# Kernel optimization log

Hardware: AMD Instinct MI355X
Metric: run time of the kernel (lower is better)

## Reference

```python
import jax, jax.numpy as jnp
import numpy as np

NEG_INF = -1e30  # stands in for -inf on the H-diagonal (matches softmax zeroing)


def conv1x1(x, W, b):
    # x: [B,C,H,W], W: [O,C], b: [O] -> [B,O,H,W]
    return jnp.einsum('bchw,oc->bohw', x, W) + b[None, :, None, None]


def setup_inputs() -> dict:
    key = jax.random.key(0)
    ks = jax.random.split(key, 8)
    B, C, H, W = 4, 64, 256, 256
    C8 = C // 8
    s = 1.0 / np.sqrt(C)
    return {
        'x': jax.random.normal(ks[0], (B, C, H, W), jnp.float32),
        'Wq': jax.random.normal(ks[1], (C8, C), jnp.float32) * s,
        'bq': jnp.zeros((C8,), jnp.float32),
        'Wk': jax.random.normal(ks[2], (C8, C), jnp.float32) * s,
        'bk': jnp.zeros((C8,), jnp.float32),
        'Wv': jax.random.normal(ks[3], (C, C), jnp.float32) * s,
        'bv': jnp.zeros((C,), jnp.float32),
        'gamma': jnp.zeros((1,), jnp.float32),
    }


def reference(x, Wq, bq, Wk, bk, Wv, bv, gamma):
    B, C, H, W = x.shape
    q = conv1x1(x, Wq, bq)   # [B,C8,H,W]
    k = conv1x1(x, Wk, bk)   # [B,C8,H,W]
    v = conv1x1(x, Wv, bv)   # [B,C,H,W]

    # Row (height-axis) attention energies with -inf on the self (diagonal) entry.
    energy_H = jnp.einsum('bchw,bcjw->bhwj', q, k)               # [B,H,W,H]
    diag = jnp.eye(H, dtype=bool)[:, None, :]                    # [H,1,H]
    energy_H = jnp.where(diag[None], NEG_INF, energy_H)
    # Column (width-axis) attention energies.
    energy_W = jnp.einsum('bchw,bchj->bhwj', q, k)               # [B,H,W,W]

    att = jax.nn.softmax(jnp.concatenate([energy_H, energy_W], axis=3), axis=3)
    att_H, att_W = att[..., :H], att[..., H:]                    # [B,H,W,H], [B,H,W,W]

    out_H = jnp.einsum('bcjw,bhwj->bchw', v, att_H)
    out_W = jnp.einsum('bchj,bhwj->bchw', v, att_W)
    return gamma[0] * (out_H + out_W) + x
```

## Files before the change

### kernel.cpp

```cpp
#include <hip/hip_runtime.h>

#define Bn 4
#define Cn 64
#define Hn 256
#define Wn 256
#define HWn 65536

typedef unsigned int u32;
typedef __attribute__((ext_vector_type(8))) short bf16x8;
typedef __attribute__((ext_vector_type(4))) float f32x4;
typedef __attribute__((ext_vector_type(16))) float f32x16;

__device__ __forceinline__ unsigned short f2b(float f) {
    union { float f; unsigned u; } v; v.f = f;
    return (unsigned short)(v.u >> 16);
}
__device__ __forceinline__ float b2f(unsigned short s) {
    union { float f; unsigned u; } v; v.u = ((unsigned)s) << 16;
    return v.f;
}
__device__ __forceinline__ u32 cvtpk(float lo, float hi) {
    u32 r;
    asm("v_cvt_pk_bf16_f32 %0, %1, %2" : "=v"(r) : "v"(lo), "v"(hi));
    return r;
}
__device__ __forceinline__ void vswap(u32& a, u32& b) {
    asm volatile("v_permlane32_swap_b32 %0, %1" : "+v"(a), "+v"(b));
}
__device__ __forceinline__ float pair_other(float v, int lane) {
    union { float f; u32 u; } A; A.f = v;
    u32 a = A.u, b = A.u;
    vswap(a, b);
    union { u32 u; float f; } R; R.u = (lane < 32) ? b : a;
    return R.f;
}
__device__ __forceinline__ bf16x8 buildP(const float* p) {
    u32 A = cvtpk(p[0], p[1]), B = cvtpk(p[4], p[5]);
    u32 C = cvtpk(p[2], p[3]), D = cvtpk(p[6], p[7]);
    vswap(A, B); vswap(C, D);
    union { u32 w[4]; bf16x8 v; } u;
    u.w[0] = A; u.w[1] = C; u.w[2] = B; u.w[3] = D;
    return u.v;
}

__global__ __launch_bounds__(256) void k_proj(
    const float* __restrict__ x,
    const float* __restrict__ Wq, const float* __restrict__ bq,
    const float* __restrict__ Wk, const float* __restrict__ bk,
    const float* __restrict__ Wv, const float* __restrict__ bv,
    unsigned short* __restrict__ qbr, unsigned short* __restrict__ kbr,
    unsigned short* __restrict__ qbT, unsigned short* __restrict__ kbT,
    unsigned short* __restrict__ v_row)
{
    int t = threadIdx.x, lane = t & 63, wv = t >> 6;
    int bid = blockIdx.x, b = bid >> 8, h = bid & 255;
    int row16 = lane & 15, g = lane >> 4;

    bf16x8 Af[5][2];
    #pragma unroll
    for (int m = 0; m < 5; ++m) {
        const float* wrow;
        if (m == 0) wrow = (row16 < 8) ? (Wq + row16 * 64) : (Wk + (row16 - 8) * 64);
        else        wrow = Wv + (size_t)((m - 1) * 16 + row16) * 64;
        #pragma unroll
        for (int ks = 0; ks < 2; ++ks) {
            int c0 = ks * 32 + g * 8;
            f32x4 w0 = *(const f32x4*)(wrow + c0);
            f32x4 w1 = *(const f32x4*)(wrow + c0 + 4);
            bf16x8 a;
            a[0] = (short)f2b(w0[0]); a[1] = (short)f2b(w0[1]);
            a[2] = (short)f2b(w0[2]); a[3] = (short)f2b(w0[3]);
            a[4] = (short)f2b(w1[0]); a[5] = (short)f2b(w1[1]);
            a[6] = (short)f2b(w1[2]); a[7] = (short)f2b(w1[3]);
            Af[m][ks] = a;
        }
    }

    f32x4 acc[5][4];
    #pragma unroll
    for (int m = 0; m < 5; ++m)
        #pragma unroll
        for (int nt = 0; nt < 4; ++nt)
            acc[m][nt] = (f32x4){0.f, 0.f, 0.f, 0.f};

    const float* xb = x + (size_t)b * Cn * HWn + (size_t)h * Wn;
    #pragma unroll
    for (int nt = 0; nt < 4; ++nt) {
        int p = wv * 64 + nt * 16 + row16;
        #pragma unroll
        for (int ks = 0; ks < 2; ++ks) {
            int c0 = ks * 32 + g * 8;
            bf16x8 bf;
            #pragma unroll
            for (int i = 0; i < 8; ++i)
                bf[i] = (short)f2b(xb[(size_t)(c0 + i) * HWn + p]);
            #pragma unroll
            for (int m = 0; m < 5; ++m)
                acc[m][nt] = __builtin_amdgcn_mfma_f32_16x16x32_bf16(Af[m][ks], bf, acc[m][nt], 0, 0, 0);
        }
    }

    f32x4 bQK = (g < 2) ? *(const f32x4*)(bq + g * 4)
                        : *(const f32x4*)(bk + (g - 2) * 4);
    #pragma unroll
    for (int nt = 0; nt < 4; ++nt) {
        int p = wv * 64 + nt * 16 + row16;
        f32x4 d = acc[0][nt];
        d[0] += bQK[0]; d[1] += bQK[1]; d[2] += bQK[2]; d[3] += bQK[3];
        u32 w0 = (u32)f2b(d[0]) | ((u32)f2b(d[1]) << 16);
        u32 w1 = (u32)f2b(d[2]) | ((u32)f2b(d[3]) << 16);
        size_t roff = ((size_t)(b * Hn + h) * Wn + p) * 8 + (size_t)((g & 1) * 4);
        size_t toff = ((size_t)(b * Wn + p) * Hn + h) * 8 + (size_t)((g & 1) * 4);
        if (g < 2) {
            *(u32*)(qbr + roff) = w0; *(u32*)(qbr + roff + 2) = w1;
            *(u32*)(qbT + toff) = w0; *(u32*)(qbT + toff + 2) = w1;
        } else {
            *(u32*)(kbr + roff) = w0; *(u32*)(kbr + roff + 2) = w1;
            *(u32*)(kbT + toff) = w0; *(u32*)(kbT + toff + 2) = w1;
        }
        #pragma unroll
        for (int m = 1; m < 5; ++m) {
            f32x4 bV = *(const f32x4*)(bv + (m - 1) * 16 + g * 4);
            unsigned short* vp = v_row + (size_t)b * Cn * HWn
                               + (size_t)((m - 1) * 16 + g * 4) * HWn
                               + (size_t)h * Wn + p;
            #pragma unroll
            for (int r = 0; r < 4; ++r)
                vp[(size_t)r * HWn] = f2b(acc[m][nt][r] + bV[r]);
        }
    }
}

__global__ __launch_bounds__(256) void k_tr_bf16(
    const unsigned short* __restrict__ in, unsigned short* __restrict__ out,
    int R, int Ccols)
{
    __shared__ unsigned short tile[64][66];
    int t = threadIdx.x;
    int lr = t >> 6, lc = t & 63;
    int tilesC = Ccols >> 6;
    int per_b = (R >> 6) * tilesC;
    int bid = blockIdx.x;
    int b = bid / per_b;
    int rem = bid - b * per_b;
    int r0 = (rem / tilesC) << 6;
    int c0 = (rem - (rem / tilesC) * tilesC) << 6;
    const unsigned short* ip = in + (size_t)b * R * Ccols;
    unsigned short* op = out + (size_t)b * R * Ccols;
    #pragma unroll
    for (int i = 0; i < 16; ++i) {
        int r = lr * 16 + i;
        tile[r][lc] = ip[(size_t)(r0 + r) * Ccols + c0 + lc];
    }
    __syncthreads();
    #pragma unroll
    for (int i = 0; i < 16; ++i) {
        int c = lr * 16 + i;
        op[(size_t)(c0 + c) * R + r0 + lc] = tile[lc][c];
    }
}

__global__ __launch_bounds__(256, 2) void k_attnH(
    const unsigned short* __restrict__ qT, const unsigned short* __restrict__ kT,
    const unsigned short* __restrict__ vT,
    unsigned short* __restrict__ ohT,
    float* __restrict__ mH, float* __restrict__ sH)
{
    __shared__ __align__(16) unsigned short Vl[16384];
    int t = threadIdx.x, lane = t & 63, wv = t >> 6;
    int l31 = lane & 31, hi = lane >> 5;
    int bid = blockIdx.x, b = bid >> 8, w = bid & 255;

    const char* vsrc = (const char*)(vT + ((size_t)(b * Wn + w)) * Cn * Hn);
    #pragma unroll
    for (int p = 0; p < 8; ++p) {
        int lin = p * 4096 + t * 16;
        int c = lin >> 9;
        f32x4 d = *(const f32x4*)(vsrc + lin);
        unsigned dst = (unsigned)lin ^ ((unsigned)(c & 7) << 4);
        *(f32x4*)((char*)Vl + dst) = d;
    }

    const unsigned short* qb = qT + ((size_t)(b * Wn + w)) * Hn * 8;
    const unsigned short* kb = kT + ((size_t)(b * Wn + w)) * Hn * 8;
    bf16x8 zer = {};
    bf16x8 Qf[2], Kf[8];
    #pragma unroll
    for (int qt = 0; qt < 2; ++qt) {
        int q = (wv * 2 + qt) * 32 + l31;
        bf16x8 v = *(const bf16x8*)(qb + (size_t)q * 8);
        Qf[qt] = (hi == 0) ? v : zer;
    }
    #pragma unroll
    for (int jt = 0; jt < 8; ++jt) {
        int j = jt * 32 + l31;
        bf16x8 v = *(const bf16x8*)(kb + (size_t)j * 8);
        Kf[jt] = (hi == 0) ? v : zer;
    }
    __syncthreads();

    #pragma unroll
    for (int qt = 0; qt < 2; ++qt) {
        int qtA = wv * 2 + qt;
        int q = qtA * 32 + l31;
        f32x16 Oa = {}, Ob = {};
        float m = -3.0e38f, s = 0.f;
        #pragma unroll
        for (int jt = 0; jt < 8; ++jt) {
            f32x16 zc = {};
            f32x16 e = __builtin_amdgcn_mfma_f32_32x32x16_bf16(Kf[jt], Qf[qt], zc, 0, 0, 0);
            if (jt == qtA) {
                #pragma unroll
                for (int r = 0; r < 16; ++r) {
                    int rl = (r & 3) + 8 * (r >> 2) + 4 * hi;
                    e[r] = (rl == l31) ? -1e30f : e[r];
                }
            }
            float pm = e[0];
            #pragma unroll
            for (int r = 1; r < 16; ++r) pm = fmaxf(pm, e[r]);
            pm = fmaxf(pm, pair_other(pm, lane));
            if (!__all(pm <= m + 8.0f)) {
                float mn = fmaxf(m, pm);
                float f = __expf(m - mn);
                #pragma unroll
                for (int r = 0; r < 16; ++r) { Oa[r] *= f; Ob[r] *= f; }
                s *= f; m = mn;
            }
            float p[16];
            float ss = 0.f;
            #pragma unroll
            for (int r = 0; r < 16; ++r) { p[r] = __expf(e[r] - m); ss += p[r]; }
            s += ss;
            bf16x8 P0 = buildP(p);
            bf16x8 P1 = buildP(p + 8);
            #pragma unroll
            for (int k2 = 0; k2 < 2; ++k2) {
                int ktA = jt * 2 + k2;
                bf16x8 Pf = k2 ? P1 : P0;
                #pragma unroll
                for (int ct = 0; ct < 2; ++ct) {
                    int c = ct * 32 + l31;
                    unsigned ad = ((unsigned)(c * 512 + ktA * 32 + hi * 16))
                                ^ ((unsigned)(c & 7) << 4);
                    bf16x8 Vf = *(const bf16x8*)((const char*)Vl + ad);
                    if (ct == 0) Oa = __builtin_amdgcn_mfma_f32_32x32x16_bf16(Vf, Pf, Oa, 0, 0, 0);
                    else         Ob = __builtin_amdgcn_mfma_f32_32x32x16_bf16(Vf, Pf, Ob, 0, 0, 0);
                }
            }
        }
        float s_tot = s + pair_other(s, lane);
        if (hi == 0) {
            size_t so = ((size_t)(b * Wn + w)) * Hn + q;
            mH[so] = m; sH[so] = s_tot;
        }
        unsigned short* ob = ohT + ((size_t)(b * Wn + w)) * Cn * Hn;
        #pragma unroll
        for (int ct = 0; ct < 2; ++ct) {
            #pragma unroll
            for (int r = 0; r < 16; ++r) {
                int c = (r & 3) + 8 * (r >> 2) + 4 * hi + ct * 32;
                float val = ct ? Ob[r] : Oa[r];
                ob[(size_t)c * Hn + q] = f2b(val);
            }
        }
    }
}

__global__ __launch_bounds__(256, 2) void k_attnW(
    const unsigned short* __restrict__ qbr, const unsigned short* __restrict__ kbr,
    const unsigned short* __restrict__ v_row,
    const unsigned short* __restrict__ oh_row,
    const float* __restrict__ mH, const float* __restrict__ sH,
    const float* __restrict__ x, const float* __restrict__ gamma,
    float* __restrict__ out)
{
    __shared__ __align__(16) unsigned short Vl[16384];
    int t = threadIdx.x, lane = t & 63, wv = t >> 6;
    int l31 = lane & 31, hi = lane >> 5;
    int bid = blockIdx.x, b = bid >> 8, h = bid & 255;

    #pragma unroll
    for (int p = 0; p < 8; ++p) {
        int lin = p * 4096 + t * 16;
        int c = lin >> 9, off = lin & 511;
        const char* src = (const char*)(v_row + ((size_t)(b * Cn + c)) * HWn + (size_t)h * Wn) + off;
        f32x4 d = *(const f32x4*)src;
        unsigned dst = (unsigned)lin ^ ((unsigned)(c & 7) << 4);
        *(f32x4*)((char*)Vl + dst) = d;
    }

    const unsigned short* qb = qbr + ((size_t)(b * Hn + h)) * Wn * 8;
    const unsigned short* kb = kbr + ((size_t)(b * Hn + h)) * Wn * 8;
    bf16x8 zer = {};
    bf16x8 Qf[2], Kf[8];
    #pragma unroll
    for (int qt = 0; qt < 2; ++qt) {
        int q = (wv * 2 + qt) * 32 + l31;
        bf16x8 v = *(const bf16x8*)(qb + (size_t)q * 8);
        Qf[qt] = (hi == 0) ? v : zer;
    }
    #pragma unroll
    for (int jt = 0; jt < 8; ++jt) {
        int j = jt * 32 + l31;
        bf16x8 v = *(const bf16x8*)(kb + (size_t)j * 8);
        Kf[jt] = (hi == 0) ? v : zer;
    }
    float g = gamma[0];
    __syncthreads();

    #pragma unroll
    for (int qt = 0; qt < 2; ++qt) {
        int q = (wv * 2 + qt) * 32 + l31;
        f32x16 Oa = {}, Ob = {};
        float m = -3.0e38f, s = 0.f;
        #pragma unroll
        for (int jt = 0; jt < 8; ++jt) {
            f32x16 zc = {};
            f32x16 e = __builtin_amdgcn_mfma_f32_32x32x16_bf16(Kf[jt], Qf[qt], zc, 0, 0, 0);
            float pm = e[0];
            #pragma unroll
            for (int r = 1; r < 16; ++r) pm = fmaxf(pm, e[r]);
            pm = fmaxf(pm, pair_other(pm, lane));
            if (!__all(pm <= m + 8.0f)) {
                float mn = fmaxf(m, pm);
                float f = __expf(m - mn);
                #pragma unroll
                for (int r = 0; r < 16; ++r) { Oa[r] *= f; Ob[r] *= f; }
                s *= f; m = mn;
            }
            float p[16];
            float ss = 0.f;
            #pragma unroll
            for (int r = 0; r < 16; ++r) { p[r] = __expf(e[r] - m); ss += p[r]; }
            s += ss;
            bf16x8 P0 = buildP(p);
            bf16x8 P1 = buildP(p + 8);
            #pragma unroll
            for (int k2 = 0; k2 < 2; ++k2) {
                int ktA = jt * 2 + k2;
                bf16x8 Pf = k2 ? P1 : P0;
                #pragma unroll
                for (int ct = 0; ct < 2; ++ct) {
                    int c = ct * 32 + l31;
                    unsigned ad = ((unsigned)(c * 512 + ktA * 32 + hi * 16))
                                ^ ((unsigned)(c & 7) << 4);
                    bf16x8 Vf = *(const bf16x8*)((const char*)Vl + ad);
                    if (ct == 0) Oa = __builtin_amdgcn_mfma_f32_32x32x16_bf16(Vf, Pf, Oa, 0, 0, 0);
                    else         Ob = __builtin_amdgcn_mfma_f32_32x32x16_bf16(Vf, Pf, Ob, 0, 0, 0);
                }
            }
        }
        float s_tot = s + pair_other(s, lane);
        size_t so = ((size_t)(b * Wn + q)) * Hn + h;
        float mh = mH[so], sh = sH[so];
        float M = fmaxf(m, mh);
        float eW = __expf(m - M), eH = __expf(mh - M);
        float inv = 1.0f / (s_tot * eW + sh * eH);
        float sI = eW * inv, sF = eH * inv;
        #pragma unroll
        for (int ct = 0; ct < 2; ++ct) {
            #pragma unroll
            for (int r = 0; r < 16; ++r) {
                int c = (r & 3) + 8 * (r >> 2) + 4 * hi + ct * 32;
                size_t idx = ((size_t)(b * Cn + c) * Hn + h) * Wn + q;
                float val = ct ? Ob[r] : Oa[r];
                out[idx] = g * (val * sI + b2f(oh_row[idx]) * sF) + x[idx];
            }
        }
    }
}

extern "C" void kernel_launch(void* const* d_in, const int* in_sizes, int n_in,
                              void* d_out, int out_size, void* d_ws, size_t ws_size,
                              hipStream_t stream) {
    const float* x  = (const float*)d_in[0];
    const float* Wq = (const float*)d_in[1];
    const float* bq = (const float*)d_in[2];
    const float* Wk = (const float*)d_in[3];
    const float* bk = (const float*)d_in[4];
    const float* Wv = (const float*)d_in[5];
    const float* bv = (const float*)d_in[6];
    const float* gm = (const float*)d_in[7];
    float* out = (float*)d_out;
    char* ws = (char*)d_ws;

    const size_t BHW = (size_t)Bn * Hn * Wn;
    unsigned short* qbr = (unsigned short*)ws;
    unsigned short* kbr = qbr + 8 * BHW;
    unsigned short* qbT = kbr + 8 * BHW;
    unsigned short* kbT = qbT + 8 * BHW;
    unsigned short* v_row = kbT + 8 * BHW;
    unsigned short* vT    = v_row + 64 * BHW;
    unsigned short* ohT   = vT + 64 * BHW;
    unsigned short* oh_row = vT;
    float* mHb = (float*)(ohT + 64 * BHW);
    float* sHb = mHb + BHW;

    k_proj<<<Bn * Hn, 256, 0, stream>>>(x, Wq, bq, Wk, bk, Wv, bv,
                                        qbr, kbr, qbT, kbT, v_row);
    k_tr_bf16<<<Bn * (16384 / 64) * (256 / 64), 256, 0, stream>>>(v_row, vT, 16384, 256);
    k_attnH<<<Bn * Wn, 256, 0, stream>>>(qbT, kbT, vT, ohT, mHb, sHb);
    k_tr_bf16<<<Bn * (256 / 64) * (16384 / 64), 256, 0, stream>>>(ohT, oh_row, 256, 16384);
    k_attnW<<<Bn * Hn, 256, 0, stream>>>(qbr, kbr, v_row, oh_row, mHb, sHb, x, gm, out);
}
```

Measured before the change: 125.0 us.

## Drop transposed Q/K copies and split projection blocks in half

The projection kernel no longer writes transposed copies of Q and K. The H-axis attention kernel now reads Q and K with a strided gather from the row-major buffers instead. The projection grid is doubled, so each block covers half a row, which gives more blocks to spread across the GPU. This removes scattered 8-byte transposed stores and their traffic, at the cost of 16-byte loads in attnH that sit a full row apart and coalesce poorly.

```diff
diff --git a/kernel.cpp b/kernel.cpp
--- a/kernel.cpp
+++ b/kernel.cpp
@@ -49,11 +49,12 @@
     const float* __restrict__ Wk, const float* __restrict__ bk,
     const float* __restrict__ Wv, const float* __restrict__ bv,
     unsigned short* __restrict__ qbr, unsigned short* __restrict__ kbr,
-    unsigned short* __restrict__ qbT, unsigned short* __restrict__ kbT,
     unsigned short* __restrict__ v_row)
 {
     int t = threadIdx.x, lane = t & 63, wv = t >> 6;
-    int bid = blockIdx.x, b = bid >> 8, h = bid & 255;
+    int bid = blockIdx.x;
+    int b = bid >> 9, rest = bid & 511;
+    int h = rest >> 1, half = rest & 1;
     int row16 = lane & 15, g = lane >> 4;
 
     bf16x8 Af[5][2];
@@ -76,17 +77,17 @@
         }
     }
 
-    f32x4 acc[5][4];
+    f32x4 acc[5][2];
     #pragma unroll
     for (int m = 0; m < 5; ++m)
         #pragma unroll
-        for (int nt = 0; nt < 4; ++nt)
+        for (int nt = 0; nt < 2; ++nt)
             acc[m][nt] = (f32x4){0.f, 0.f, 0.f, 0.f};
 
     const float* xb = x + (size_t)b * Cn * HWn + (size_t)h * Wn;
     #pragma unroll
-    for (int nt = 0; nt < 4; ++nt) {
-        int p = wv * 64 + nt * 16 + row16;
+    for (int nt = 0; nt < 2; ++nt) {
+        int p = half * 128 + wv * 32 + nt * 16 + row16;
         #pragma unroll
         for (int ks = 0; ks < 2; ++ks) {
             int c0 = ks * 32 + g * 8;
@@ -103,20 +104,17 @@
     f32x4 bQK = (g < 2) ? *(const f32x4*)(bq + g * 4)
                         : *(const f32x4*)(bk + (g - 2) * 4);
     #pragma unroll
-    for (int nt = 0; nt < 4; ++nt) {
-        int p = wv * 64 + nt * 16 + row16;
+    for (int nt = 0; nt < 2; ++nt) {
+        int p = half * 128 + wv * 32 + nt * 16 + row16;
         f32x4 d = acc[0][nt];
         d[0] += bQK[0]; d[1] += bQK[1]; d[2] += bQK[2]; d[3] += bQK[3];
         u32 w0 = (u32)f2b(d[0]) | ((u32)f2b(d[1]) << 16);
         u32 w1 = (u32)f2b(d[2]) | ((u32)f2b(d[3]) << 16);
         size_t roff = ((size_t)(b * Hn + h) * Wn + p) * 8 + (size_t)((g & 1) * 4);
-        size_t toff = ((size_t)(b * Wn + p) * Hn + h) * 8 + (size_t)((g & 1) * 4);
         if (g < 2) {
             *(u32*)(qbr + roff) = w0; *(u32*)(qbr + roff + 2) = w1;
-            *(u32*)(qbT + toff) = w0; *(u32*)(qbT + toff + 2) = w1;
         } else {
             *(u32*)(kbr + roff) = w0; *(u32*)(kbr + roff + 2) = w1;
-            *(u32*)(kbT + toff) = w0; *(u32*)(kbT + toff + 2) = w1;
         }
         #pragma unroll
         for (int m = 1; m < 5; ++m) {
@@ -161,7 +159,7 @@
 }
 
 __global__ __launch_bounds__(256, 2) void k_attnH(
-    const unsigned short* __restrict__ qT, const unsigned short* __restrict__ kT,
+    const unsigned short* __restrict__ qbr, const unsigned short* __restrict__ kbr,
     const unsigned short* __restrict__ vT,
     unsigned short* __restrict__ ohT,
     float* __restrict__ mH, float* __restrict__ sH)
@@ -181,20 +179,18 @@
         *(f32x4*)((char*)Vl + dst) = d;
     }
 
-    const unsigned short* qb = qT + ((size_t)(b * Wn + w)) * Hn * 8;
-    const unsigned short* kb = kT + ((size_t)(b * Wn + w)) * Hn * 8;
     bf16x8 zer = {};
     bf16x8 Qf[2], Kf[8];
     #pragma unroll
     for (int qt = 0; qt < 2; ++qt) {
         int q = (wv * 2 + qt) * 32 + l31;
-        bf16x8 v = *(const bf16x8*)(qb + (size_t)q * 8);
+        bf16x8 v = *(const bf16x8*)(qbr + ((size_t)(b * Hn + q) * Wn + w) * 8);
         Qf[qt] = (hi == 0) ? v : zer;
     }
     #pragma unroll
     for (int jt = 0; jt < 8; ++jt) {
         int j = jt * 32 + l31;
-        bf16x8 v = *(const bf16x8*)(kb + (size_t)j * 8);
+        bf16x8 v = *(const bf16x8*)(kbr + ((size_t)(b * Hn + j) * Wn + w) * 8);
         Kf[jt] = (hi == 0) ? v : zer;
     }
     __syncthreads();
@@ -388,19 +384,17 @@
     const size_t BHW = (size_t)Bn * Hn * Wn;
     unsigned short* qbr = (unsigned short*)ws;
     unsigned short* kbr = qbr + 8 * BHW;
-    unsigned short* qbT = kbr + 8 * BHW;
-    unsigned short* kbT = qbT + 8 * BHW;
-    unsigned short* v_row = kbT + 8 * BHW;
+    unsigned short* v_row = kbr + 8 * BHW;
     unsigned short* vT    = v_row + 64 * BHW;
     unsigned short* ohT   = vT + 64 * BHW;
     unsigned short* oh_row = vT;
     float* mHb = (float*)(ohT + 64 * BHW);
     float* sHb = mHb + BHW;
 
-    k_proj<<<Bn * Hn, 256, 0, stream>>>(x, Wq, bq, Wk, bk, Wv, bv,
-                                        qbr, kbr, qbT, kbT, v_row);
+    k_proj<<<Bn * Hn * 2, 256, 0, stream>>>(x, Wq, bq, Wk, bk, Wv, bv,
+                                            qbr, kbr, v_row);
     k_tr_bf16<<<Bn * (16384 / 64) * (256 / 64), 256, 0, stream>>>(v_row, vT, 16384, 256);
-    k_attnH<<<Bn * Wn, 256, 0, stream>>>(qbT, kbT, vT, ohT, mHb, sHb);
+    k_attnH<<<Bn * Wn, 256, 0, stream>>>(qbr, kbr, vT, ohT, mHb, sHb);
     k_tr_bf16<<<Bn * (256 / 64) * (16384 / 64), 256, 0, stream>>>(ohT, oh_row, 256, 16384);
     k_attnW<<<Bn * Hn, 256, 0, stream>>>(qbr, kbr, v_row, oh_row, mHb, sHb, x, gm, out);
 }
```

New measurement: 125.7 us. No clear change (+0.5%).
